# Optimization experiments

Hardware: AMD Instinct MI355X
Metric: run time of the kernel (lower is better)

The kernel has to match this reference:

```python
import jax, jax.numpy as jnp
import numpy as np

WIN = 9
EPS = 1e-06

def _box_conv(x, win):
    C = x.shape[1]
    k = jnp.ones((C, C, win, win), dtype=x.dtype)
    pad = win // 2
    return jax.lax.conv_general_dilated(
        x, k, window_strides=(1, 1), padding=[(pad, pad), (pad, pad)],
        dimension_numbers=('NCHW', 'OIHW', 'NCHW'))

def setup_inputs() -> dict:
    key = jax.random.key(0)
    k1, k2 = jax.random.split(key)
    shape = (32, 1, 512, 512)
    template = jax.random.uniform(k1, shape, dtype=jnp.float32)
    image = jax.random.uniform(k2, shape, dtype=jnp.float32)
    return {"template": template, "image": image}

def reference(template, image):
    I2 = template * template
    J2 = image * image
    IJ = image * template

    I_sum = _box_conv(template, WIN)
    J_sum = _box_conv(image, WIN)
    I2_sum = _box_conv(I2, WIN)
    J2_sum = _box_conv(J2, WIN)
    IJ_sum = _box_conv(IJ, WIN)

    win_area = float(WIN * WIN)
    u_I = I_sum / win_area
    u_J = J_sum / win_area

    cross = IJ_sum - u_J * I_sum - u_I * J_sum + u_I * u_J * win_area
    I_var = I2_sum - 2.0 * u_I * I_sum + u_I * u_I * win_area
    J_var = J2_sum - 2.0 * u_J * J_sum + u_J * u_J * win_area

    scores = cross / (jnp.sqrt(I_var) * jnp.sqrt(J_var) + EPS)
    return 1.0 - jnp.mean(scores)
```

## Files before the change

kernel.cpp:

```cpp
#include <hip/hip_runtime.h>
#include <math.h>

#define IMG    512
#define IMG2   (IMG*IMG)
#define TC     64
#define TR     32
#define ECC    72
#define PITCH  33
#define NBATCH 32
#define NBLOCKS ((IMG/TC)*(IMG/TR)*NBATCH)
#define NPIX   8388608.0f

typedef unsigned int u32;

__device__ __forceinline__ u32 pk_bf16(float a, float b) {
    float r;
    asm("v_cvt_pk_bf16_f32 %0, %1, %2" : "=v"(r) : "v"(a), "v"(b));
    return __float_as_uint(r);
}
__device__ __forceinline__ float lo16(u32 x) { return __uint_as_float(x << 16); }
__device__ __forceinline__ float hi16(u32 x) { return __uint_as_float(x & 0xffff0000u); }

__global__ __launch_bounds__(256, 5)
void lncc_main(const float* __restrict__ Tm, const float* __restrict__ Im,
               float* __restrict__ partial)
{
    __shared__ uint2 AB[ECC * PITCH];
    __shared__ u32   Cc[ECC * PITCH];
    __shared__ float wsum[4];

    const int tid = threadIdx.x;
    const int x0 = blockIdx.x * TC;
    const int y0 = blockIdx.y * TR;
    const size_t base = (size_t)blockIdx.z * IMG2;
    const float* tb = Tm + base;
    const float* ib = Im + base;

    const bool interior = (blockIdx.x - 1u < 6u) & (blockIdx.y - 1u < 14u);

    if (tid < 3 * ECC) {
        const int ec    = tid % ECC;
        const int strip = tid / ECC;
        const int r0    = strip * 11;

        float tv_[19], vv_[19];

        if (interior) {
            const int off0 = (y0 + r0 - 4) * IMG + (x0 + ec - 4);
            const float* tp = tb + off0;
            const float* ip = ib + off0;
            #pragma unroll
            for (int j = 0; j < 19; ++j) {
                tv_[j] = tp[j * IMG];
                vv_[j] = ip[j * IMG];
            }
        } else {
            const int gx   = x0 + ec - 4;
            const float xm = ((unsigned)gx < IMG) ? 1.0f : 0.0f;
            const int gxc  = gx < 0 ? 0 : (gx > IMG - 1 ? IMG - 1 : gx);
            const int Y    = y0 + r0 - 4;
            #pragma unroll
            for (int j = 0; j < 19; ++j) {
                const int gy  = Y + j;
                const float m = ((unsigned)gy < IMG) ? xm : 0.0f;
                const int gyc = gy < 0 ? 0 : (gy > IMG - 1 ? IMG - 1 : gy);
                const int off = (gyc << 9) + gxc;
                tv_[j] = tb[off] * m;
                vv_[j] = ib[off] * m;
            }
        }

        float s0 = 0.f, s1 = 0.f, s2 = 0.f, s3 = 0.f, s4 = 0.f;
        #pragma unroll
        for (int j = 0; j < 19; ++j) {
            const float t = tv_[j], v = vv_[j];
            s0 += t; s1 += v;
            s2 = fmaf(t, t, s2); s3 = fmaf(v, v, s3); s4 = fmaf(t, v, s4);
            if (j >= 8) {
                const int idx = ec * PITCH + r0 + (j - 8);
                AB[idx] = make_uint2(pk_bf16(s0, s1), pk_bf16(s2, s3));
                Cc[idx] = pk_bf16(s4, s4);
                const float ot = tv_[j - 8], ov = vv_[j - 8];
                s0 -= ot; s1 -= ov;
                s2 = fmaf(-ot, ot, s2); s3 = fmaf(-ov, ov, s3); s4 = fmaf(-ot, ov, s4);
            }
        }
    }
    __syncthreads();

    float lsum = 0.f;
    {
        const int row = tid & 31;
        const int b0  = (tid >> 5) * 8 * PITCH + row;
        float W0 = 0.f, W1 = 0.f, W2 = 0.f, W3 = 0.f, W4 = 0.f;
        float r0_[9], r1_[9], r2_[9], r3_[9], r4_[9];
        const float inv81 = 1.0f / 81.0f;

        #pragma unroll
        for (int k = 0; k < 16; ++k) {
            const uint2 ab = AB[b0 + k * PITCH];
            const u32   c  = Cc[b0 + k * PITCH];
            const float h0 = lo16(ab.x), h1 = hi16(ab.x);
            const float h2 = lo16(ab.y), h3 = hi16(ab.y);
            const float h4 = hi16(c);
            W0 += h0; W1 += h1; W2 += h2; W3 += h3; W4 += h4;
            const int ri = k % 9;
            r0_[ri] = h0; r1_[ri] = h1; r2_[ri] = h2; r3_[ri] = h3; r4_[ri] = h4;
            if (k >= 8) {
                const float t0 = W0 * inv81;
                const float t1 = W1 * inv81;
                const float cross = fmaf(-t0, W1, W4);
                const float Iv    = fmaf(-t0, W0, W2);
                const float Jv    = fmaf(-t1, W1, W3);
                const float den   = fmaf(Iv, Jv, 1e-12f);
                lsum = fmaf(cross, __builtin_amdgcn_rsqf(den), lsum);
                const int o = (k - 8) % 9;
                W0 -= r0_[o]; W1 -= r1_[o]; W2 -= r2_[o]; W3 -= r3_[o]; W4 -= r4_[o];
            }
        }
    }

    #pragma unroll
    for (int d = 32; d >= 1; d >>= 1) lsum += __shfl_down(lsum, d, 64);
    if ((tid & 63) == 0) wsum[tid >> 6] = lsum;
    __syncthreads();
    if (tid == 0) {
        const int bid = (blockIdx.z * gridDim.y + blockIdx.y) * gridDim.x + blockIdx.x;
        partial[bid] = wsum[0] + wsum[1] + wsum[2] + wsum[3];
    }
}

__global__ __launch_bounds__(256)
void lncc_reduce(const float* __restrict__ partial, float* __restrict__ out)
{
    __shared__ float ws[4];
    const int tid = threadIdx.x;
    float s = 0.f;
    #pragma unroll
    for (int i = 0; i < NBLOCKS / 256; ++i) s += partial[tid + i * 256];
    #pragma unroll
    for (int d = 32; d >= 1; d >>= 1) s += __shfl_down(s, d, 64);
    if ((tid & 63) == 0) ws[tid >> 6] = s;
    __syncthreads();
    if (tid == 0) out[0] = 1.0f - (ws[0] + ws[1] + ws[2] + ws[3]) / NPIX;
}

extern "C" void kernel_launch(void* const* d_in, const int* in_sizes, int n_in,
                              void* d_out, int out_size, void* d_ws, size_t ws_size,
                              hipStream_t stream)
{
    (void)in_sizes; (void)n_in; (void)out_size; (void)ws_size;
    const float* Tm = (const float*)d_in[0];
    const float* Im = (const float*)d_in[1];
    float* out  = (float*)d_out;
    float* part = (float*)d_ws;

    dim3 grid(IMG / TC, IMG / TR, NBATCH);
    lncc_main<<<grid, 256, 0, stream>>>(Tm, Im, part);
    lncc_reduce<<<1, 256, 0, stream>>>(part, out);
}
```

Measured before the change: 27.41 us.

## Fuse final reduction into main kernel via atomic counter and packed-f32 window math

Removes the separate reduce kernel launch by appending one extra block that spins on a global atomic counter until all tile blocks have published their partial sums, then reduces them. Tile blocks now write partials atomically and bump the counter. A memset is added to clear the counter each call. The vertical sliding-window arithmetic is also rewritten with 2-wide float vectors so the compiler can emit packed FP32 ops. The spin-wait block assumes forward progress of the other blocks and adds a memset op in place of the second launch.

```diff
diff --git a/kernel.cpp b/kernel.cpp
--- a/kernel.cpp
+++ b/kernel.cpp
@@ -7,11 +7,11 @@
 #define TR     32
 #define ECC    72
 #define PITCH  33
-#define NBATCH 32
-#define NBLOCKS ((IMG/TC)*(IMG/TR)*NBATCH)
+#define NTILES 4096
 #define NPIX   8388608.0f
 
 typedef unsigned int u32;
+typedef float f2 __attribute__((ext_vector_type(2)));
 
 __device__ __forceinline__ u32 pk_bf16(float a, float b) {
     float r;
@@ -23,20 +23,45 @@
 
 __global__ __launch_bounds__(256, 5)
 void lncc_main(const float* __restrict__ Tm, const float* __restrict__ Im,
-               float* __restrict__ partial)
+               float* __restrict__ ws, float* __restrict__ out)
 {
+    u32*   cnt     = (u32*)ws;
+    float* partial = ws + 64;
+
     __shared__ uint2 AB[ECC * PITCH];
     __shared__ u32   Cc[ECC * PITCH];
     __shared__ float wsum[4];
 
     const int tid = threadIdx.x;
-    const int x0 = blockIdx.x * TC;
-    const int y0 = blockIdx.y * TR;
-    const size_t base = (size_t)blockIdx.z * IMG2;
+    const int bid = blockIdx.x;
+
+    if (bid == NTILES) {
+        if (tid == 0) {
+            while (atomicAdd(cnt, 0u) < NTILES) __builtin_amdgcn_s_sleep(8);
+        }
+        __syncthreads();
+        float s = 0.f;
+        #pragma unroll
+        for (int i = 0; i < NTILES / 256; ++i)
+            s += atomicAdd(&partial[tid + i * 256], 0.0f);
+        #pragma unroll
+        for (int d = 32; d >= 1; d >>= 1) s += __shfl_down(s, d, 64);
+        if ((tid & 63) == 0) wsum[tid >> 6] = s;
+        __syncthreads();
+        if (tid == 0) out[0] = 1.0f - (wsum[0] + wsum[1] + wsum[2] + wsum[3]) / NPIX;
+        return;
+    }
+
+    const int bx = bid & 7;
+    const int by = (bid >> 3) & 15;
+    const int bz = bid >> 7;
+    const int x0 = bx * TC;
+    const int y0 = by * TR;
+    const size_t base = (size_t)bz * IMG2;
     const float* tb = Tm + base;
     const float* ib = Im + base;
 
-    const bool interior = (blockIdx.x - 1u < 6u) & (blockIdx.y - 1u < 14u);
+    const bool interior = ((unsigned)(bx - 1) < 6u) & ((unsigned)(by - 1) < 14u);
 
     if (tid < 3 * ECC) {
         const int ec    = tid % ECC;
@@ -92,30 +117,31 @@
     {
         const int row = tid & 31;
         const int b0  = (tid >> 5) * 8 * PITCH + row;
-        float W0 = 0.f, W1 = 0.f, W2 = 0.f, W3 = 0.f, W4 = 0.f;
-        float r0_[9], r1_[9], r2_[9], r3_[9], r4_[9];
-        const float inv81 = 1.0f / 81.0f;
+        f2 W01 = {0.f, 0.f}, W23 = {0.f, 0.f};
+        float W4 = 0.f;
+        f2 r01[9], r23[9];
+        float r4[9];
+        const f2 inv81 = {1.0f / 81.0f, 1.0f / 81.0f};
 
         #pragma unroll
         for (int k = 0; k < 16; ++k) {
             const uint2 ab = AB[b0 + k * PITCH];
             const u32   c  = Cc[b0 + k * PITCH];
-            const float h0 = lo16(ab.x), h1 = hi16(ab.x);
-            const float h2 = lo16(ab.y), h3 = hi16(ab.y);
+            f2 h01, h23;
+            h01.x = lo16(ab.x); h01.y = hi16(ab.x);
+            h23.x = lo16(ab.y); h23.y = hi16(ab.y);
             const float h4 = hi16(c);
-            W0 += h0; W1 += h1; W2 += h2; W3 += h3; W4 += h4;
+            W01 += h01; W23 += h23; W4 += h4;
             const int ri = k % 9;
-            r0_[ri] = h0; r1_[ri] = h1; r2_[ri] = h2; r3_[ri] = h3; r4_[ri] = h4;
+            r01[ri] = h01; r23[ri] = h23; r4[ri] = h4;
             if (k >= 8) {
-                const float t0 = W0 * inv81;
-                const float t1 = W1 * inv81;
-                const float cross = fmaf(-t0, W1, W4);
-                const float Iv    = fmaf(-t0, W0, W2);
-                const float Jv    = fmaf(-t1, W1, W3);
-                const float den   = fmaf(Iv, Jv, 1e-12f);
+                const f2 tt  = W01 * inv81;
+                const f2 IJv = W23 - tt * W01;
+                const float cross = fmaf(-tt.x, W01.y, W4);
+                const float den   = fmaf(IJv.x, IJv.y, 1e-12f);
                 lsum = fmaf(cross, __builtin_amdgcn_rsqf(den), lsum);
                 const int o = (k - 8) % 9;
-                W0 -= r0_[o]; W1 -= r1_[o]; W2 -= r2_[o]; W3 -= r3_[o]; W4 -= r4_[o];
+                W01 -= r01[o]; W23 -= r23[o]; W4 -= r4[o];
             }
         }
     }
@@ -125,24 +151,11 @@
     if ((tid & 63) == 0) wsum[tid >> 6] = lsum;
     __syncthreads();
     if (tid == 0) {
-        const int bid = (blockIdx.z * gridDim.y + blockIdx.y) * gridDim.x + blockIdx.x;
-        partial[bid] = wsum[0] + wsum[1] + wsum[2] + wsum[3];
+        const float bsum = wsum[0] + wsum[1] + wsum[2] + wsum[3];
+        atomicExch(&partial[bid], bsum);
+        asm volatile("s_waitcnt vmcnt(0)" ::: "memory");
+        atomicAdd(cnt, 1u);
     }
-}
-
-__global__ __launch_bounds__(256)
-void lncc_reduce(const float* __restrict__ partial, float* __restrict__ out)
-{
-    __shared__ float ws[4];
-    const int tid = threadIdx.x;
-    float s = 0.f;
-    #pragma unroll
-    for (int i = 0; i < NBLOCKS / 256; ++i) s += partial[tid + i * 256];
-    #pragma unroll
-    for (int d = 32; d >= 1; d >>= 1) s += __shfl_down(s, d, 64);
-    if ((tid & 63) == 0) ws[tid >> 6] = s;
-    __syncthreads();
-    if (tid == 0) out[0] = 1.0f - (ws[0] + ws[1] + ws[2] + ws[3]) / NPIX;
 }
 
 extern "C" void kernel_launch(void* const* d_in, const int* in_sizes, int n_in,
@@ -152,10 +165,9 @@
     (void)in_sizes; (void)n_in; (void)out_size; (void)ws_size;
     const float* Tm = (const float*)d_in[0];
     const float* Im = (const float*)d_in[1];
-    float* out  = (float*)d_out;
-    float* part = (float*)d_ws;
+    float* ws  = (float*)d_ws;
+    float* out = (float*)d_out;
 
-    dim3 grid(IMG / TC, IMG / TR, NBATCH);
-    lncc_main<<<grid, 256, 0, stream>>>(Tm, Im, part);
-    lncc_reduce<<<1, 256, 0, stream>>>(part, out);
+    hipMemsetAsync(d_ws, 0, 4, stream);
+    lncc_main<<<NTILES + 1, 256, 0, stream>>>(Tm, Im, ws, out);
 }
```

Result: slower. 67.65 us (+146.8%).
